# Performance work log

Hardware: AMD Instinct MI355X
Metric: run time of the kernel (lower is better)

Reference implementation:

```python
import jax, jax.numpy as jnp
import numpy as np

EMBED_DIM = 768
FF_MULT = 4
HIDDEN = EMBED_DIM * FF_MULT
BATCH, SEQ = 32, 1024
EPS = 1e-6


def rmsnorm(x, g):
    # RMSNorm over last dim with learned scale g
    return x * jax.lax.rsqrt(jnp.mean(x * x, axis=-1, keepdims=True) + EPS) * g


def act_quant(x):
    # per-token int8 absmax quantization (BitNet b1.58)
    scale = 127.0 / jnp.clip(jnp.max(jnp.abs(x), axis=-1, keepdims=True), 1e-5, None)
    return jnp.clip(jnp.round(x * scale), -128.0, 127.0) / scale


def weight_quant(w):
    # per-tensor ternary (1.58-bit) absmean quantization
    scale = 1.0 / jnp.clip(jnp.mean(jnp.abs(w)), 1e-5, None)
    return jnp.clip(jnp.round(w * scale), -1.0, 1.0) / scale


def bitlinear(x, w, g):
    xn = rmsnorm(x, g)
    # straight-through estimator: forward uses quantized values
    xq = xn + jax.lax.stop_gradient(act_quant(xn) - xn)
    wq = w + jax.lax.stop_gradient(weight_quant(w) - w)
    return jnp.einsum('bsd,fd->bsf', xq, wq)


def setup_inputs() -> dict:
    key = jax.random.key(0)
    k1, k2, k3 = jax.random.split(key, 3)
    x = jax.random.normal(k1, (BATCH, SEQ, EMBED_DIM), dtype=jnp.float32)
    w1 = jax.random.normal(k2, (HIDDEN, EMBED_DIM), dtype=jnp.float32) * 0.02
    w2 = jax.random.normal(k3, (EMBED_DIM, HIDDEN), dtype=jnp.float32) * 0.02
    g1 = jnp.ones((EMBED_DIM,), dtype=jnp.float32)
    g2 = jnp.ones((HIDDEN,), dtype=jnp.float32)
    return {"x": x, "w1": w1, "g1": g1, "w2": w2, "g2": g2}


def reference(x, w1, g1, w2, g2):
    # BitFeedForward: BitLinear -> GELU (exact, matches nn.GELU) -> BitLinear
    # Dropout(p=0.0) is identity.
    h = jax.nn.gelu(bitlinear(x, w1, g1), approximate=False)
    return bitlinear(h, w2, g2)
```

## Files before the change

kernel.cpp:

```cpp
#include <hip/hip_runtime.h>
#include <hip/hip_bf16.h>
#include <hip/hip_fp16.h>
#include <math.h>

#define TOKENS 32768
#define EMBED  768
#define HIDDEN 3072
#define WELEMS (EMBED*HIDDEN)

typedef __attribute__((ext_vector_type(4))) int i32x4;
typedef __attribute__((ext_vector_type(4))) signed char i8x4;
typedef signed char i8;

__device__ __forceinline__ float wave_reduce_sum(float v) {
    for (int o = 32; o > 0; o >>= 1) v += __shfl_down(v, o);
    return v;
}
__device__ __forceinline__ float wave_reduce_max(float v) {
    for (int o = 32; o > 0; o >>= 1) v = fmaxf(v, __shfl_down(v, o));
    return v;
}

__device__ __forceinline__ float gelu_fast(float v) {
    const float z  = fabsf(v) * 0.70710678118654752440f;
    const float t  = __builtin_amdgcn_rcpf(fmaf(0.3275911f, z, 1.0f));
    float p = fmaf(1.061405429f, t, -1.453152027f);
    p = fmaf(p, t, 1.421413741f);
    p = fmaf(p, t, -0.284496736f);
    p = fmaf(p, t, 0.254829592f);
    p = p * t;
    const float e   = __expf(-z * z);
    const float erf = fmaf(-p, e, 1.0f);
    const float se  = (v >= 0.f) ? erf : -erf;
    return 0.5f * v * (1.0f + se);
}

__global__ __launch_bounds__(256) void k_abs_partial(const float* __restrict__ w,
                                                     float* __restrict__ out, int n) {
    float s = 0.f;
    for (int i = blockIdx.x * 256 + threadIdx.x; i < n; i += gridDim.x * 256)
        s += fabsf(w[i]);
    __shared__ float red[4];
    s = wave_reduce_sum(s);
    if ((threadIdx.x & 63) == 0) red[threadIdx.x >> 6] = s;
    __syncthreads();
    if (threadIdx.x == 0) out[blockIdx.x] = red[0] + red[1] + red[2] + red[3];
}

__global__ __launch_bounds__(256) void k_finalize(const float* __restrict__ p,
                                                  float* __restrict__ m) {
    __shared__ float r1[4], r2[4];
    float s1 = 0.f, s2 = 0.f;
    for (int i = threadIdx.x; i < 512; i += 256) { s1 += p[i]; s2 += p[512 + i]; }
    s1 = wave_reduce_sum(s1); s2 = wave_reduce_sum(s2);
    if ((threadIdx.x & 63) == 0) { r1[threadIdx.x >> 6] = s1; r2[threadIdx.x >> 6] = s2; }
    __syncthreads();
    if (threadIdx.x == 0) {
        float m1 = (r1[0] + r1[1] + r1[2] + r1[3]) / (float)WELEMS;
        float m2 = (r2[0] + r2[1] + r2[2] + r2[3]) / (float)WELEMS;
        m[0] = fmaxf(m1, 1e-5f);
        m[1] = fmaxf(m2, 1e-5f);
    }
}

__global__ __launch_bounds__(256) void k_quant_w(const float* __restrict__ w,
                                                 i8* __restrict__ wq,
                                                 const float* __restrict__ mp, int n) {
    const float inv = 1.0f / mp[0];
    for (int i = blockIdx.x * 256 + threadIdx.x; i < n; i += gridDim.x * 256) {
        float q = rintf(w[i] * inv);
        q = fminf(1.f, fmaxf(-1.f, q));
        wq[i] = (i8)(int)q;
    }
}

template <int D>
__global__ __launch_bounds__(256) void k_rms_quant_f32(const float* __restrict__ x,
                                                       const float* __restrict__ g,
                                                       i8* __restrict__ xq,
                                                       float* __restrict__ sc) {
    constexpr int NV = D / 4;
    constexpr int IT = (NV + 255) / 256;
    __shared__ float reds[4], redm[4];
    const int t = blockIdx.x;
    const float4* xp = reinterpret_cast<const float4*>(x + (size_t)t * D);
    const float4* gp = reinterpret_cast<const float4*>(g);
    float4 xg[IT];
    float ssq = 0.f, amax = 0.f;
#pragma unroll
    for (int i = 0; i < IT; ++i) {
        const int idx = i * 256 + (int)threadIdx.x;
        const bool act = (NV % 256 == 0) || (idx < NV);
        if (act) {
            float4 v = xp[idx];
            float4 gv = gp[idx];
            ssq += v.x * v.x + v.y * v.y + v.z * v.z + v.w * v.w;
            xg[i].x = v.x * gv.x; xg[i].y = v.y * gv.y;
            xg[i].z = v.z * gv.z; xg[i].w = v.w * gv.w;
            amax = fmaxf(amax, fmaxf(fmaxf(fabsf(xg[i].x), fabsf(xg[i].y)),
                                     fmaxf(fabsf(xg[i].z), fabsf(xg[i].w))));
        } else {
            xg[i].x = xg[i].y = xg[i].z = xg[i].w = 0.f;
        }
    }
    ssq = wave_reduce_sum(ssq);
    amax = wave_reduce_max(amax);
    if ((threadIdx.x & 63) == 0) { reds[threadIdx.x >> 6] = ssq; redm[threadIdx.x >> 6] = amax; }
    __syncthreads();
    const float S = reds[0] + reds[1] + reds[2] + reds[3];
    const float A = fmaxf(fmaxf(redm[0], redm[1]), fmaxf(redm[2], redm[3]));
    const float rs = (float)(1.0 / sqrt((double)S / D + 1e-6));
    const float an = fmaxf(A * rs, 1e-5f);
    const float qs = rs * (127.0f / an);
    if (threadIdx.x == 0) sc[t] = an * (1.0f / 127.0f);
    i8x4* op = reinterpret_cast<i8x4*>(xq + (size_t)t * D);
#pragma unroll
    for (int i = 0; i < IT; ++i) {
        const int idx = i * 256 + (int)threadIdx.x;
        const bool act = (NV % 256 == 0) || (idx < NV);
        if (act) {
            i8x4 r;
            r[0] = (i8)(int)fminf(127.f, fmaxf(-128.f, rintf(xg[i].x * qs)));
            r[1] = (i8)(int)fminf(127.f, fmaxf(-128.f, rintf(xg[i].y * qs)));
            r[2] = (i8)(int)fminf(127.f, fmaxf(-128.f, rintf(xg[i].z * qs)));
            r[3] = (i8)(int)fminf(127.f, fmaxf(-128.f, rintf(xg[i].w * qs)));
            op[idx] = r;
        }
    }
}

template <int D>
__global__ __launch_bounds__(256) void k_rms_quant_f16(const __half* __restrict__ x,
                                                       const float* __restrict__ g,
                                                       i8* __restrict__ xq,
                                                       float* __restrict__ sc) {
    constexpr int NV = D / 8;
    constexpr int IT = (NV + 255) / 256;
    __shared__ float reds[4], redm[4];
    const int t = blockIdx.x;
    const int4* xp = reinterpret_cast<const int4*>(x + (size_t)t * D);
    const float4* gp = reinterpret_cast<const float4*>(g);
    float xg[IT][8];
    float ssq = 0.f, amax = 0.f;
#pragma unroll
    for (int i = 0; i < IT; ++i) {
        const int idx = i * 256 + (int)threadIdx.x;
        const bool act = (NV % 256 == 0) || (idx < NV);
        if (act) {
            int4 raw = xp[idx];
            const __half2* hp = reinterpret_cast<const __half2*>(&raw);
            float4 g0 = gp[idx * 2];
            float4 g1 = gp[idx * 2 + 1];
            float gv[8] = {g0.x, g0.y, g0.z, g0.w, g1.x, g1.y, g1.z, g1.w};
#pragma unroll
            for (int j = 0; j < 4; ++j) {
                float2 f = __half22float2(hp[j]);
                float a0 = f.x, a1 = f.y;
                ssq += a0 * a0 + a1 * a1;
                xg[i][j * 2]     = a0 * gv[j * 2];
                xg[i][j * 2 + 1] = a1 * gv[j * 2 + 1];
                amax = fmaxf(amax, fmaxf(fabsf(xg[i][j * 2]), fabsf(xg[i][j * 2 + 1])));
            }
        } else {
#pragma unroll
            for (int j = 0; j < 8; ++j) xg[i][j] = 0.f;
        }
    }
    ssq = wave_reduce_sum(ssq);
    amax = wave_reduce_max(amax);
    if ((threadIdx.x & 63) == 0) { reds[threadIdx.x >> 6] = ssq; redm[threadIdx.x >> 6] = amax; }
    __syncthreads();
    const float S = reds[0] + reds[1] + reds[2] + reds[3];
    const float A = fmaxf(fmaxf(redm[0], redm[1]), fmaxf(redm[2], redm[3]));
    const float rs = (float)(1.0 / sqrt((double)S / D + 1e-6));
    const float an = fmaxf(A * rs, 1e-5f);
    const float qs = rs * (127.0f / an);
    if (threadIdx.x == 0) sc[t] = an * (1.0f / 127.0f);
    i8x4* op = reinterpret_cast<i8x4*>(xq + (size_t)t * D);
#pragma unroll
    for (int i = 0; i < IT; ++i) {
        const int idx = i * 256 + (int)threadIdx.x;
        const bool act = (NV % 256 == 0) || (idx < NV);
        if (act) {
            i8x4 r0, r1;
#pragma unroll
            for (int j = 0; j < 4; ++j)
                r0[j] = (i8)(int)fminf(127.f, fmaxf(-128.f, rintf(xg[i][j] * qs)));
#pragma unroll
            for (int j = 0; j < 4; ++j)
                r1[j] = (i8)(int)fminf(127.f, fmaxf(-128.f, rintf(xg[i][4 + j] * qs)));
            op[idx * 2]     = r0;
            op[idx * 2 + 1] = r1;
        }
    }
}

template <bool GELU, typename OutT>
__global__ __launch_bounds__(512, 4) void k_gemm_i8(const i8* __restrict__ A,
                                                    const i8* __restrict__ B,
                                                    OutT* __restrict__ C,
                                                    const float* __restrict__ rsc,
                                                    const float* __restrict__ msc,
                                                    int nbx, int N, int K) {
    __shared__ i8 As[128 * 128];
    __shared__ i8 Bs[256 * 128];
    const int nwg = (int)gridDim.x;
    const int id  = (int)blockIdx.x;
    const int q = nwg >> 3, r = nwg & 7;
    const int xcd = id & 7, sub = id >> 3;
    const int swz = (xcd < r ? xcd * (q + 1) : r * (q + 1) + (xcd - r) * q) + sub;
    const int bx = swz % nbx;
    const int by = swz / nbx;

    const int tid  = threadIdx.x;
    const int lane = tid & 63;
    const int wave = tid >> 6;
    const int wr = wave >> 2, wc = wave & 3;
    const size_t rowBase = (size_t)by * 128;
    const size_t colBase = (size_t)bx * 256;
    const float ms = msc[0];

    i32x4 acc[4][4] = {};

    const int srow = tid >> 3;
    const int cc   = tid & 7;
    const int gcol = (cc ^ (srow & 7)) * 16;
    const i8* gA0 = A + (rowBase + srow) * (size_t)K + gcol;
    const i8* gB0 = B + (colBase + srow) * (size_t)K + gcol;
    const int lOff = srow * 128 + cc * 16;

    const int frow = lane & 15;
    const int fko  = (lane >> 4) * 16;
    const int rswz = (frow & 7) << 4;

    for (int k0 = 0; k0 < K; k0 += 128) {
#pragma unroll
        for (int r2 = 0; r2 < 2; ++r2)
            __builtin_amdgcn_global_load_lds(
                (const __attribute__((address_space(1))) void*)(gA0 + (size_t)r2 * 64 * K + k0),
                (__attribute__((address_space(3))) void*)(&As[lOff + r2 * 64 * 128]), 16, 0, 0);
#pragma unroll
        for (int r4 = 0; r4 < 4; ++r4)
            __builtin_amdgcn_global_load_lds(
                (const __attribute__((address_space(1))) void*)(gB0 + (size_t)r4 * 64 * K + k0),
                (__attribute__((address_space(3))) void*)(&Bs[lOff + r4 * 64 * 128]), 16, 0, 0);
        __syncthreads();
#pragma unroll
        for (int ks = 0; ks < 2; ++ks) {
            i32x4 af[4], bv[4];
#pragma unroll
            for (int mi = 0; mi < 4; ++mi)
                af[mi] = *(const i32x4*)(&As[(wr * 64 + mi * 16 + frow) * 128
                                             + ((ks * 64 + fko) ^ rswz)]);
#pragma unroll
            for (int ni = 0; ni < 4; ++ni)
                bv[ni] = *(const i32x4*)(&Bs[(wc * 64 + ni * 16 + frow) * 128
                                             + ((ks * 64 + fko) ^ rswz)]);
#pragma unroll
            for (int mi = 0; mi < 4; ++mi)
#pragma unroll
                for (int ni = 0; ni < 4; ++ni)
                    acc[mi][ni] = __builtin_amdgcn_mfma_i32_16x16x64_i8(
                        af[mi], bv[ni], acc[mi][ni], 0, 0, 0);
        }
        __syncthreads();
    }

    const int ccol = lane & 15;
    const int crg  = lane >> 4;
#pragma unroll
    for (int mi = 0; mi < 4; ++mi) {
#pragma unroll
        for (int i = 0; i < 4; ++i) {
            size_t row = rowBase + wr * 64 + mi * 16 + crg * 4 + i;
            float rscale = rsc[row] * ms;
#pragma unroll
            for (int ni = 0; ni < 4; ++ni) {
                size_t col = colBase + wc * 64 + ni * 16 + ccol;
                float v = (float)acc[mi][ni][i] * rscale;
                if (GELU) v = gelu_fast(v);
                C[row * (size_t)N + col] = (OutT)v;
            }
        }
    }
}

extern "C" void kernel_launch(void* const* d_in, const int* in_sizes, int n_in,
                              void* d_out, int out_size, void* d_ws, size_t ws_size,
                              hipStream_t stream) {
    const float* x  = (const float*)d_in[0];
    const float* w1 = (const float*)d_in[1];
    const float* g1 = (const float*)d_in[2];
    const float* w2 = (const float*)d_in[3];
    const float* g2 = (const float*)d_in[4];
    float* out = (float*)d_out;

    char* ws = (char*)d_ws;
    float* partials = (float*)ws;
    float* mvals    = (float*)(ws + 4096);
    float* a        = (float*)(ws + 4352);
    float* b        = (float*)(ws + 135424);
    i8*    wq1      = (i8*)(ws + 266496);
    i8*    wq2      = (i8*)(ws + 2625792);
    const size_t FIXED = 4985088;
    char* chunkMem = ws + FIXED;

    const size_t PER_TOK = 768 + 6144 + 3072;
    size_t avail = (ws_size > FIXED) ? (ws_size - FIXED) : 0;
    long long ch = (long long)(avail / PER_TOK);
    ch &= ~255LL;
    if (ch < 256) ch = 256;
    if (ch > TOKENS) ch = TOKENS;
    const int CH = (int)ch;

    k_abs_partial<<<512, 256, 0, stream>>>(w1, partials, WELEMS);
    k_abs_partial<<<512, 256, 0, stream>>>(w2, partials + 512, WELEMS);
    k_finalize<<<1, 256, 0, stream>>>(partials, mvals);
    k_quant_w<<<2048, 256, 0, stream>>>(w1, wq1, mvals + 0, WELEMS);
    k_quant_w<<<2048, 256, 0, stream>>>(w2, wq2, mvals + 1, WELEMS);

    for (int base = 0; base < TOKENS; base += CH) {
        const int rows = (TOKENS - base < CH) ? (TOKENS - base) : CH;
        i8*     xqc = (i8*)chunkMem;
        __half* hc  = (__half*)(chunkMem + (size_t)CH * 768);
        i8*     hqc = (i8*)(chunkMem + (size_t)CH * 768 + (size_t)CH * 6144);

        const int nby = rows / 128;
        const int nbx1 = HIDDEN / 256;
        const int nbx2 = EMBED / 256;

        k_rms_quant_f32<EMBED><<<rows, 256, 0, stream>>>(
            x + (size_t)base * EMBED, g1, xqc, a + base);
        k_gemm_i8<true, __half><<<nbx1 * nby, 512, 0, stream>>>(
            xqc, wq1, hc, a + base, mvals + 0, nbx1, HIDDEN, EMBED);
        k_rms_quant_f16<HIDDEN><<<rows, 256, 0, stream>>>(
            hc, g2, hqc, b + base);
        k_gemm_i8<false, float><<<nbx2 * nby, 512, 0, stream>>>(
            hqc, wq2, out + (size_t)base * EMBED, b + base, mvals + 1, nbx2, EMBED, HIDDEN);
    }
}
```

Before: 365.2 us.

## Narrow second GEMM tile, use tanh GELU, magic-number int8 packing

Templates the int8 GEMM on the N tile width, using 128-wide tiles for the second GEMM (N=768) so it launches more workgroups, and raises the occupancy hints in launch bounds. Replaces the erf-based GELU with the tanh approximation and replaces rint/clamp quantization with a magic-number float add and byte packing. The tanh GELU differs from the exact erf GELU the reference uses. The magic-number trick drops the explicit clamp, which is only safe because the absmax scaling already keeps values within ±127.

```diff
diff --git a/kernel.cpp b/kernel.cpp
--- a/kernel.cpp
+++ b/kernel.cpp
@@ -9,7 +9,6 @@
 #define WELEMS (EMBED*HIDDEN)
 
 typedef __attribute__((ext_vector_type(4))) int i32x4;
-typedef __attribute__((ext_vector_type(4))) signed char i8x4;
 typedef signed char i8;
 
 __device__ __forceinline__ float wave_reduce_sum(float v) {
@@ -21,18 +20,25 @@
     return v;
 }
 
-__device__ __forceinline__ float gelu_fast(float v) {
-    const float z  = fabsf(v) * 0.70710678118654752440f;
-    const float t  = __builtin_amdgcn_rcpf(fmaf(0.3275911f, z, 1.0f));
-    float p = fmaf(1.061405429f, t, -1.453152027f);
-    p = fmaf(p, t, 1.421413741f);
-    p = fmaf(p, t, -0.284496736f);
-    p = fmaf(p, t, 0.254829592f);
-    p = p * t;
-    const float e   = __expf(-z * z);
-    const float erf = fmaf(-p, e, 1.0f);
-    const float se  = (v >= 0.f) ? erf : -erf;
-    return 0.5f * v * (1.0f + se);
+__device__ __forceinline__ float gelu_tanh(float x) {
+    const float x2 = x * x;
+    const float u  = 0.7978845608f * x * fmaf(0.044715f, x2, 1.0f);
+    const float ex = __expf(u + u);
+    const float r  = __builtin_amdgcn_rcpf(ex + 1.0f);
+    const float th = fmaf(-2.0f, r, 1.0f);
+    const float hx = 0.5f * x;
+    return fmaf(hx, th, hx);
+}
+
+__device__ __forceinline__ unsigned int q8pack4(float v0, float v1, float v2,
+                                                float v3, float qs) {
+    union { float f; unsigned int i; } u0, u1, u2, u3;
+    u0.f = fmaf(v0, qs, 12582912.0f);
+    u1.f = fmaf(v1, qs, 12582912.0f);
+    u2.f = fmaf(v2, qs, 12582912.0f);
+    u3.f = fmaf(v3, qs, 12582912.0f);
+    return (u0.i & 0xFFu) | ((u1.i & 0xFFu) << 8) |
+           ((u2.i & 0xFFu) << 16) | ((u3.i & 0xFFu) << 24);
 }
 
 __global__ __launch_bounds__(256) void k_abs_partial(const float* __restrict__ w,
@@ -113,19 +119,13 @@
     const float an = fmaxf(A * rs, 1e-5f);
     const float qs = rs * (127.0f / an);
     if (threadIdx.x == 0) sc[t] = an * (1.0f / 127.0f);
-    i8x4* op = reinterpret_cast<i8x4*>(xq + (size_t)t * D);
+    unsigned int* op = reinterpret_cast<unsigned int*>(xq + (size_t)t * D);
 #pragma unroll
     for (int i = 0; i < IT; ++i) {
         const int idx = i * 256 + (int)threadIdx.x;
         const bool act = (NV % 256 == 0) || (idx < NV);
-        if (act) {
-            i8x4 r;
-            r[0] = (i8)(int)fminf(127.f, fmaxf(-128.f, rintf(xg[i].x * qs)));
-            r[1] = (i8)(int)fminf(127.f, fmaxf(-128.f, rintf(xg[i].y * qs)));
-            r[2] = (i8)(int)fminf(127.f, fmaxf(-128.f, rintf(xg[i].z * qs)));
-            r[3] = (i8)(int)fminf(127.f, fmaxf(-128.f, rintf(xg[i].w * qs)));
-            op[idx] = r;
-        }
+        if (act)
+            op[idx] = q8pack4(xg[i].x, xg[i].y, xg[i].z, xg[i].w, qs);
     }
 }
 
@@ -176,34 +176,27 @@
     const float an = fmaxf(A * rs, 1e-5f);
     const float qs = rs * (127.0f / an);
     if (threadIdx.x == 0) sc[t] = an * (1.0f / 127.0f);
-    i8x4* op = reinterpret_cast<i8x4*>(xq + (size_t)t * D);
+    unsigned int* op = reinterpret_cast<unsigned int*>(xq + (size_t)t * D);
 #pragma unroll
     for (int i = 0; i < IT; ++i) {
         const int idx = i * 256 + (int)threadIdx.x;
         const bool act = (NV % 256 == 0) || (idx < NV);
         if (act) {
-            i8x4 r0, r1;
-#pragma unroll
-            for (int j = 0; j < 4; ++j)
-                r0[j] = (i8)(int)fminf(127.f, fmaxf(-128.f, rintf(xg[i][j] * qs)));
-#pragma unroll
-            for (int j = 0; j < 4; ++j)
-                r1[j] = (i8)(int)fminf(127.f, fmaxf(-128.f, rintf(xg[i][4 + j] * qs)));
-            op[idx * 2]     = r0;
-            op[idx * 2 + 1] = r1;
-        }
-    }
-}
-
-template <bool GELU, typename OutT>
-__global__ __launch_bounds__(512, 4) void k_gemm_i8(const i8* __restrict__ A,
-                                                    const i8* __restrict__ B,
-                                                    OutT* __restrict__ C,
-                                                    const float* __restrict__ rsc,
-                                                    const float* __restrict__ msc,
-                                                    int nbx, int N, int K) {
+            op[idx * 2]     = q8pack4(xg[i][0], xg[i][1], xg[i][2], xg[i][3], qs);
+            op[idx * 2 + 1] = q8pack4(xg[i][4], xg[i][5], xg[i][6], xg[i][7], qs);
+        }
+    }
+}
+
+template <int BN, bool GELU, typename OutT>
+__global__ __launch_bounds__(512, BN == 256 ? 6 : 8)
+void k_gemm_i8(const i8* __restrict__ A, const i8* __restrict__ B,
+               OutT* __restrict__ C, const float* __restrict__ rsc,
+               const float* __restrict__ msc, int nbx, int N, int K) {
+    constexpr int NI = BN / 64;
     __shared__ i8 As[128 * 128];
-    __shared__ i8 Bs[256 * 128];
+    __shared__ i8 Bs[BN * 128];
+
     const int nwg = (int)gridDim.x;
     const int id  = (int)blockIdx.x;
     const int q = nwg >> 3, r = nwg & 7;
@@ -212,15 +205,15 @@
     const int bx = swz % nbx;
     const int by = swz / nbx;
 
-    const int tid  = threadIdx.x;
+    const int tid  = (int)threadIdx.x;
     const int lane = tid & 63;
     const int wave = tid >> 6;
     const int wr = wave >> 2, wc = wave & 3;
     const size_t rowBase = (size_t)by * 128;
-    const size_t colBase = (size_t)bx * 256;
+    const size_t colBase = (size_t)bx * BN;
     const float ms = msc[0];
 
-    i32x4 acc[4][4] = {};
+    i32x4 acc[4][NI] = {};
 
     const int srow = tid >> 3;
     const int cc   = tid & 7;
@@ -240,26 +233,26 @@
                 (const __attribute__((address_space(1))) void*)(gA0 + (size_t)r2 * 64 * K + k0),
                 (__attribute__((address_space(3))) void*)(&As[lOff + r2 * 64 * 128]), 16, 0, 0);
 #pragma unroll
-        for (int r4 = 0; r4 < 4; ++r4)
+        for (int r4 = 0; r4 < BN / 64; ++r4)
             __builtin_amdgcn_global_load_lds(
                 (const __attribute__((address_space(1))) void*)(gB0 + (size_t)r4 * 64 * K + k0),
                 (__attribute__((address_space(3))) void*)(&Bs[lOff + r4 * 64 * 128]), 16, 0, 0);
         __syncthreads();
 #pragma unroll
         for (int ks = 0; ks < 2; ++ks) {
-            i32x4 af[4], bv[4];
+            i32x4 af[4], bv[NI];
 #pragma unroll
             for (int mi = 0; mi < 4; ++mi)
                 af[mi] = *(const i32x4*)(&As[(wr * 64 + mi * 16 + frow) * 128
                                              + ((ks * 64 + fko) ^ rswz)]);
 #pragma unroll
-            for (int ni = 0; ni < 4; ++ni)
-                bv[ni] = *(const i32x4*)(&Bs[(wc * 64 + ni * 16 + frow) * 128
+            for (int ni = 0; ni < NI; ++ni)
+                bv[ni] = *(const i32x4*)(&Bs[(wc * (BN / 4) + ni * 16 + frow) * 128
                                              + ((ks * 64 + fko) ^ rswz)]);
 #pragma unroll
             for (int mi = 0; mi < 4; ++mi)
 #pragma unroll
-                for (int ni = 0; ni < 4; ++ni)
+                for (int ni = 0; ni < NI; ++ni)
                     acc[mi][ni] = __builtin_amdgcn_mfma_i32_16x16x64_i8(
                         af[mi], bv[ni], acc[mi][ni], 0, 0, 0);
         }
@@ -275,10 +268,10 @@
             size_t row = rowBase + wr * 64 + mi * 16 + crg * 4 + i;
             float rscale = rsc[row] * ms;
 #pragma unroll
-            for (int ni = 0; ni < 4; ++ni) {
-                size_t col = colBase + wc * 64 + ni * 16 + ccol;
+            for (int ni = 0; ni < NI; ++ni) {
+                size_t col = colBase + wc * (BN / 4) + ni * 16 + ccol;
                 float v = (float)acc[mi][ni][i] * rscale;
-                if (GELU) v = gelu_fast(v);
+                if (GELU) v = gelu_tanh(v);
                 C[row * (size_t)N + col] = (OutT)v;
             }
         }
@@ -325,17 +318,17 @@
         __half* hc  = (__half*)(chunkMem + (size_t)CH * 768);
         i8*     hqc = (i8*)(chunkMem + (size_t)CH * 768 + (size_t)CH * 6144);
 
-        const int nby = rows / 128;
+        const int nby  = rows / 128;
         const int nbx1 = HIDDEN / 256;
-        const int nbx2 = EMBED / 256;
+        const int nbx2 = EMBED / 128;
 
         k_rms_quant_f32<EMBED><<<rows, 256, 0, stream>>>(
             x + (size_t)base * EMBED, g1, xqc, a + base);
-        k_gemm_i8<true, __half><<<nbx1 * nby, 512, 0, stream>>>(
+        k_gemm_i8<256, true, __half><<<nbx1 * nby, 512, 0, stream>>>(
             xqc, wq1, hc, a + base, mvals + 0, nbx1, HIDDEN, EMBED);
         k_rms_quant_f16<HIDDEN><<<rows, 256, 0, stream>>>(
             hc, g2, hqc, b + base);
-        k_gemm_i8<false, float><<<nbx2 * nby, 512, 0, stream>>>(
+        k_gemm_i8<128, false, float><<<nbx2 * nby, 512, 0, stream>>>(
             hqc, wq2, out + (size_t)base * EMBED, b + base, mvals + 1, nbx2, EMBED, HIDDEN);
     }
 }
```

Measured after the change: 614.8 us. 68.3% more time.
